# Kernel tuning notes

Hardware: AMD Instinct MI355X
Metric: run time of the kernel (lower is better)

The kernel has to match this reference:

```python
import jax, jax.numpy as jnp
import numpy as np

HEADS = 8
DIM_HEAD = 64
QUERY_DIM = 512
INNER = HEADS * DIM_HEAD
DIAG_OFFSET = 1
T_TEMP = 1.0
NEG_INF = -1e9  # used via -inf below; kept for clarity


def setup_inputs() -> dict:
    key = jax.random.key(0)
    ks = jax.random.split(key, 8)
    b, s, f = 2, 2048, 16
    x = jax.random.normal(ks[0], (b, s, f, QUERY_DIM), dtype=jnp.float32)
    pos_bias = jax.random.normal(ks[1], (HEADS, f, f), dtype=jnp.float32)
    w_scale = 0.02
    Wq = jax.random.normal(ks[2], (QUERY_DIM, INNER), dtype=jnp.float32) * w_scale
    Wk = jax.random.normal(ks[3], (QUERY_DIM, INNER), dtype=jnp.float32) * w_scale
    Wv = jax.random.normal(ks[4], (QUERY_DIM, INNER), dtype=jnp.float32) * w_scale
    Wo = jax.random.normal(ks[5], (INNER, QUERY_DIM), dtype=jnp.float32) * w_scale
    bo = jax.random.normal(ks[6], (QUERY_DIM,), dtype=jnp.float32) * w_scale
    return {"x": x, "pos_bias": pos_bias, "Wq": Wq, "Wk": Wk, "Wv": Wv, "Wo": Wo, "bo": bo}


def reference(x, pos_bias, Wq, Wk, Wv, Wo, bo):
    # x: [b, s, f, c] -- temporal attention over the frame axis f per spatial token
    b, s, f, _ = x.shape
    scale = DIM_HEAD ** -0.5
    q = (x @ Wq).reshape(b, s, f, HEADS, DIM_HEAD)
    k = (x @ Wk).reshape(b, s, f, HEADS, DIM_HEAD)
    v = (x @ Wv).reshape(b, s, f, HEADS, DIM_HEAD)
    # scores over frames: [b, s, h, f_q, f_k]
    w = jnp.einsum('bsihd,bsjhd->bshij', q * scale, k)
    w = w + pos_bias[None, None]  # [h, f, f] relative position bias
    # attend_prev_only causal mask (strict, diag_offset=1)
    causal = jnp.triu(jnp.ones((f, f), dtype=jnp.float32), k=DIAG_OFFSET)
    w = w + jnp.where(causal == 1.0, -jnp.inf, 0.0)
    # faithful to source: subtract row max, then softmax with temperature
    w = w - jax.lax.stop_gradient(jnp.max(w, axis=-1, keepdims=True))
    p = jax.nn.softmax(w.astype(jnp.float32) / T_TEMP, axis=-1).astype(w.dtype)
    out = jnp.einsum('bshij,bsjhd->bsihd', p, v).reshape(b, s, f, INNER)
    return out @ Wo + bo
```

## Files before the change

kernel.cpp:

```cpp
#include <hip/hip_runtime.h>

typedef unsigned short u16;
typedef __attribute__((ext_vector_type(8))) unsigned short u16x8;
typedef __attribute__((ext_vector_type(8))) __bf16 bf16x8;
typedef __attribute__((ext_vector_type(4))) float f32x4;

#define M_ROWS 65536
#define KDIM   512
#define NKT    8

typedef __attribute__((address_space(1))) const void gconst_void;
typedef __attribute__((address_space(3))) void lds_void;

static __device__ __forceinline__ u16 f2bf(float f) {
  unsigned u = __builtin_bit_cast(unsigned, f);
  u += 0x7FFFu + ((u >> 16) & 1u);
  return (u16)(u >> 16);
}

static __device__ __forceinline__ f32x4 mfma_bf16(u16x8 a, u16x8 b, f32x4 c) {
  return __builtin_amdgcn_mfma_f32_16x16x32_bf16(
      __builtin_bit_cast(bf16x8, a), __builtin_bit_cast(bf16x8, b), c, 0, 0, 0);
}

__global__ void conv_x(const float* __restrict__ x, u16* __restrict__ xb) {
  const size_t t = (size_t)blockIdx.x * 256 + threadIdx.x;
  f32x4 a = *(const f32x4*)(x + t * 8);
  f32x4 b = *(const f32x4*)(x + t * 8 + 4);
  u16x8 w;
#pragma unroll
  for (int e = 0; e < 4; ++e) { w[e] = f2bf(a[e]); w[e + 4] = f2bf(b[e]); }
  *(u16x8*)(xb + t * 8) = w;
}

__global__ void convW_qkv_t(const float* __restrict__ Wq, const float* __restrict__ Wk,
                            const float* __restrict__ Wv, u16* __restrict__ Wt) {
  __shared__ float tile[32][33];
  const int bn = blockIdx.x * 32;
  const int bk = blockIdx.y * 32;
  const int tx = threadIdx.x & 31, ty = threadIdx.x >> 5;
  const float* W = (bn < 512) ? Wq : ((bn < 1024) ? Wk : Wv);
  const int coln = bn & 511;
#pragma unroll
  for (int r = 0; r < 32; r += 8)
    tile[ty + r][tx] = W[(size_t)(bk + ty + r) * 512 + coln + tx];
  __syncthreads();
#pragma unroll
  for (int r = 0; r < 32; r += 8)
    Wt[(size_t)(bn + ty + r) * 512 + bk + tx] = f2bf(tile[tx][ty + r]);
}

__global__ void convWo_t(const float* __restrict__ Wo, u16* __restrict__ Wt) {
  __shared__ float tile[32][33];
  const int bn = blockIdx.x * 32;
  const int bk = blockIdx.y * 32;
  const int tx = threadIdx.x & 31, ty = threadIdx.x >> 5;
#pragma unroll
  for (int r = 0; r < 32; r += 8)
    tile[ty + r][tx] = Wo[(size_t)(bk + ty + r) * 512 + bn + tx];
  __syncthreads();
#pragma unroll
  for (int r = 0; r < 32; r += 8)
    Wt[(size_t)(bn + ty + r) * 512 + bk + tx] = f2bf(tile[tx][ty + r]);
}

__global__ __launch_bounds__(512, 4)
void gemm_qkv_attn(const u16* __restrict__ A, const u16* __restrict__ Wt,
                   const float* __restrict__ pos_bias, u16* __restrict__ attnbuf) {
  __shared__ __attribute__((aligned(16))) u16 smem[40960];
  u16* Ab   = smem;
  u16* Bb   = smem + 16384;
  u16* qkvT = smem;
  u16* Pl   = smem + 25600;

  const int tid  = threadIdx.x;
  const int lane = tid & 63;
  const int wid  = tid >> 6;
  const int wm   = wid >> 2;
  const int wn   = wid & 3;
  const int lg   = lane >> 4;
  const int lc   = lane & 15;
  const int srow = lane >> 3;
  const int sg   = (lane & 7) ^ srow;

  const int nwg  = gridDim.x;
  const int cpx  = nwg >> 3;
  const int flat = blockIdx.x;
  const int swz  = (flat & 7) * cpx + (flat >> 3);
  const int mt   = swz >> 3;
  const int h    = swz & 7;
  const int row0 = mt * 128;

  auto stageA = [&](int buf, int unit, int kt) {
    const int rl = unit * 64 + wid * 8;
    const u16* src = A + (size_t)(row0 + rl + srow) * KDIM + kt * 64 + sg * 8;
    __builtin_amdgcn_global_load_lds((gconst_void*)src,
                                     (lds_void*)&Ab[buf * 8192 + rl * 64], 16, 0, 0);
  };
  auto stageB = [&](int buf, int unit, int kt) {
    const int rl = unit * 64 + wid * 8;
    const int grow = unit * 512 + h * 64 + wid * 8 + srow;
    const u16* src = Wt + (size_t)grow * KDIM + kt * 64 + sg * 8;
    __builtin_amdgcn_global_load_lds((gconst_void*)src,
                                     (lds_void*)&Bb[buf * 12288 + rl * 64], 16, 0, 0);
  };

  f32x4 acc[4][3];
#pragma unroll
  for (int mi = 0; mi < 4; ++mi)
#pragma unroll
    for (int ni = 0; ni < 3; ++ni) acc[mi][ni] = (f32x4){0.f, 0.f, 0.f, 0.f};

  stageA(0, 0, 0); stageA(0, 1, 0);
  stageB(0, 0, 0); stageB(0, 1, 0); stageB(0, 2, 0);
  asm volatile("s_waitcnt vmcnt(0)" ::: "memory");
  __builtin_amdgcn_s_barrier();

  for (int t = 0; t < NKT; ++t) {
    const int  c   = t & 1;
    const bool pre = (t + 1) < NKT;

    if (pre) {
      stageA(c ^ 1, 0, t + 1); stageA(c ^ 1, 1, t + 1);
      stageB(c ^ 1, 0, t + 1); stageB(c ^ 1, 1, t + 1); stageB(c ^ 1, 2, t + 1);
    }

#pragma unroll
    for (int ks = 0; ks < 2; ++ks) {
      const int gsw = ((ks * 4 + lg) ^ (lc & 7)) << 3;
      u16x8 bfr[3], af[4];
#pragma unroll
      for (int ni = 0; ni < 3; ++ni)
        bfr[ni] = *(const u16x8*)&Bb[c * 12288 + (wn * 48 + ni * 16 + lc) * 64 + gsw];
#pragma unroll
      for (int i = 0; i < 4; ++i)
        af[i] = *(const u16x8*)&Ab[c * 8192 + (wm * 64 + i * 16 + lc) * 64 + gsw];
#pragma unroll
      for (int i = 0; i < 4; ++i)
#pragma unroll
        for (int ni = 0; ni < 3; ++ni)
          acc[i][ni] = mfma_bf16(af[i], bfr[ni], acc[i][ni]);
    }

    asm volatile("s_waitcnt vmcnt(0)" ::: "memory");
    __builtin_amdgcn_s_barrier();
  }

#pragma unroll
  for (int mi = 0; mi < 4; ++mi)
#pragma unroll
    for (int ni = 0; ni < 3; ++ni) {
      const int col = wn * 48 + ni * 16 + lc;
      const int rb  = wm * 64 + mi * 16 + lg * 4;
#pragma unroll
      for (int r = 0; r < 4; ++r)
        qkvT[(rb + r) * 200 + col] = f2bf(acc[mi][ni][r]);
    }
  __syncthreads();

  const float scale = 0.125f;
  const f32x4 zf = {0.f, 0.f, 0.f, 0.f};
  const int rb = wid * 16;
  const int qb = (rb + lc) * 200;

  u16x8 aq0 = *(const u16x8*)&qkvT[qb + 0  + lg * 8];
  u16x8 aq1 = *(const u16x8*)&qkvT[qb + 32 + lg * 8];
  u16x8 bk0 = *(const u16x8*)&qkvT[qb + 64 + lg * 8];
  u16x8 bk1 = *(const u16x8*)&qkvT[qb + 96 + lg * 8];
  f32x4 s = mfma_bf16(aq0, bk0, zf);
  s = mfma_bf16(aq1, bk1, s);

  const int pb = wid * 256;
#pragma unroll
  for (int r = 0; r < 4; ++r) {
    const int i = lg * 4 + r;
    float sv = s[r] * scale + pos_bias[h * 256 + i * 16 + lc];
    if (lc > i) sv = -1e30f;
    float m = sv;
#pragma unroll
    for (int off = 8; off >= 1; off >>= 1) m = fmaxf(m, __shfl_xor(m, off));
    float e = __expf(sv - m);
    float sm = e;
#pragma unroll
    for (int off = 8; off >= 1; off >>= 1) sm += __shfl_xor(sm, off);
    Pl[pb + i * 16 + lc] = f2bf(e / sm);
  }
  asm volatile("s_waitcnt lgkmcnt(0)" ::: "memory");

  u16x8 ap = {0, 0, 0, 0, 0, 0, 0, 0};
  if (lane < 32) ap = *(const u16x8*)&Pl[pb + lc * 16 + lg * 8];

#pragma unroll
  for (int nd = 0; nd < 4; ++nd) {
    u16x8 bv = {0, 0, 0, 0, 0, 0, 0, 0};
    if (lane < 32) {
#pragma unroll
      for (int jj = 0; jj < 8; ++jj) {
        const int j = lg * 8 + jj;
        bv[jj] = qkvT[(rb + j) * 200 + 128 + nd * 16 + lc];
      }
    }
    f32x4 o = mfma_bf16(ap, bv, zf);
#pragma unroll
    for (int r = 0; r < 4; ++r) {
      const int i = lg * 4 + r;
      attnbuf[(size_t)(row0 + rb + i) * 512 + h * 64 + nd * 16 + lc] = f2bf(o[r]);
    }
  }
}

__global__ __launch_bounds__(512, 4)
void gemm_out(const u16* __restrict__ A, const u16* __restrict__ Bt,
              float* __restrict__ C, const float* __restrict__ bias) {
  __shared__ __attribute__((aligned(16))) u16 smem[32768];
  u16* Ab = smem;
  u16* Bb = smem + 16384;

  const int tid  = threadIdx.x;
  const int lane = tid & 63;
  const int wid  = tid >> 6;
  const int wm   = wid >> 2;
  const int wn   = wid & 3;
  const int lg   = lane >> 4;
  const int lc   = lane & 15;
  const int srow = lane >> 3;
  const int sg   = (lane & 7) ^ srow;

  const int nwg  = gridDim.x;
  const int cpx  = nwg >> 3;
  const int flat = blockIdx.x;
  const int swz  = (flat & 7) * cpx + (flat >> 3);
  const int mt   = swz >> 2;
  const int nt   = swz & 3;
  const int row0 = mt * 128, col0 = nt * 128;

  auto stageA = [&](int buf, int unit, int kt) {
    const int rl = unit * 64 + wid * 8;
    const u16* src = A + (size_t)(row0 + rl + srow) * KDIM + kt * 64 + sg * 8;
    __builtin_amdgcn_global_load_lds((gconst_void*)src,
                                     (lds_void*)&Ab[buf * 8192 + rl * 64], 16, 0, 0);
  };
  auto stageB = [&](int buf, int unit, int kt) {
    const int rl = unit * 64 + wid * 8;
    const u16* src = Bt + (size_t)(col0 + rl + srow) * KDIM + kt * 64 + sg * 8;
    __builtin_amdgcn_global_load_lds((gconst_void*)src,
                                     (lds_void*)&Bb[buf * 8192 + rl * 64], 16, 0, 0);
  };

  f32x4 acc[4][2];
#pragma unroll
  for (int mi = 0; mi < 4; ++mi)
#pragma unroll
    for (int ni = 0; ni < 2; ++ni) acc[mi][ni] = (f32x4){0.f, 0.f, 0.f, 0.f};

  stageA(0, 0, 0); stageA(0, 1, 0);
  stageB(0, 0, 0); stageB(0, 1, 0);
  asm volatile("s_waitcnt vmcnt(0)" ::: "memory");
  __builtin_amdgcn_s_barrier();

  for (int t = 0; t < NKT; ++t) {
    const int  c   = t & 1;
    const bool pre = (t + 1) < NKT;

    if (pre) {
      stageA(c ^ 1, 0, t + 1); stageA(c ^ 1, 1, t + 1);
      stageB(c ^ 1, 0, t + 1); stageB(c ^ 1, 1, t + 1);
    }

#pragma unroll
    for (int ks = 0; ks < 2; ++ks) {
      const int gsw = ((ks * 4 + lg) ^ (lc & 7)) << 3;
      u16x8 bfr[2], af[4];
#pragma unroll
      for (int ni = 0; ni < 2; ++ni)
        bfr[ni] = *(const u16x8*)&Bb[c * 8192 + (wn * 32 + ni * 16 + lc) * 64 + gsw];
#pragma unroll
      for (int i = 0; i < 4; ++i)
        af[i] = *(const u16x8*)&Ab[c * 8192 + (wm * 64 + i * 16 + lc) * 64 + gsw];
#pragma unroll
      for (int i = 0; i < 4; ++i)
#pragma unroll
        for (int ni = 0; ni < 2; ++ni)
          acc[i][ni] = mfma_bf16(af[i], bfr[ni], acc[i][ni]);
    }

    asm volatile("s_waitcnt vmcnt(0)" ::: "memory");
    __builtin_amdgcn_s_barrier();
  }

  const int gmb = row0 + wm * 64;
  const int gnb = col0 + wn * 32;
#pragma unroll
  for (int mi = 0; mi < 4; ++mi)
#pragma unroll
    for (int ni = 0; ni < 2; ++ni) {
      const int gm = gmb + mi * 16 + lg * 4;
      const int gn = gnb + ni * 16 + lc;
      const float bv = bias[gn];
      f32x4 v = acc[mi][ni];
#pragma unroll
      for (int r = 0; r < 4; ++r) C[(size_t)(gm + r) * 512 + gn] = v[r] + bv;
    }
}

extern "C" void kernel_launch(void* const* d_in, const int* in_sizes, int n_in,
                              void* d_out, int out_size, void* d_ws, size_t ws_size,
                              hipStream_t stream) {
  const float* x        = (const float*)d_in[0];
  const float* pos_bias = (const float*)d_in[1];
  const float* Wq       = (const float*)d_in[2];
  const float* Wk       = (const float*)d_in[3];
  const float* Wv       = (const float*)d_in[4];
  const float* Wo       = (const float*)d_in[5];
  const float* bo       = (const float*)d_in[6];
  float* out            = (float*)d_out;

  u16* xb      = (u16*)d_ws;
  u16* attnbuf = xb + (size_t)M_ROWS * 512;
  u16* Wo_t    = attnbuf + (size_t)M_ROWS * 512;
  u16* Wqkv_t  = (u16*)d_out;

  conv_x<<<dim3(M_ROWS * KDIM / (256 * 8)), dim3(256), 0, stream>>>(x, xb);
  convW_qkv_t<<<dim3(48, 16), dim3(256), 0, stream>>>(Wq, Wk, Wv, Wqkv_t);
  gemm_qkv_attn<<<dim3(4096), dim3(512), 0, stream>>>(xb, Wqkv_t, pos_bias, attnbuf);
  convWo_t<<<dim3(16, 16), dim3(256), 0, stream>>>(Wo, Wo_t);
  gemm_out<<<dim3(2048), dim3(512), 0, stream>>>(attnbuf, Wo_t, out, bo);
}
```

Baseline: 210.5 us.

## Load weight fragments directly from global memory instead of staging in LDS

```diff
diff --git a/kernel.cpp b/kernel.cpp
--- a/kernel.cpp
+++ b/kernel.cpp
@@ -67,9 +67,8 @@
 __global__ __launch_bounds__(512, 4)
 void gemm_qkv_attn(const u16* __restrict__ A, const u16* __restrict__ Wt,
                    const float* __restrict__ pos_bias, u16* __restrict__ attnbuf) {
-  __shared__ __attribute__((aligned(16))) u16 smem[40960];
+  __shared__ __attribute__((aligned(16))) u16 smem[27648];
   u16* Ab   = smem;
-  u16* Bb   = smem + 16384;
   u16* qkvT = smem;
   u16* Pl   = smem + 25600;
 
@@ -97,13 +96,14 @@
     __builtin_amdgcn_global_load_lds((gconst_void*)src,
                                      (lds_void*)&Ab[buf * 8192 + rl * 64], 16, 0, 0);
   };
-  auto stageB = [&](int buf, int unit, int kt) {
-    const int rl = unit * 64 + wid * 8;
-    const int grow = unit * 512 + h * 64 + wid * 8 + srow;
-    const u16* src = Wt + (size_t)grow * KDIM + kt * 64 + sg * 8;
-    __builtin_amdgcn_global_load_lds((gconst_void*)src,
-                                     (lds_void*)&Bb[buf * 12288 + rl * 64], 16, 0, 0);
-  };
+
+  const u16* Bw[3];
+#pragma unroll
+  for (int ni = 0; ni < 3; ++ni) {
+    const int n    = wn * 48 + ni * 16 + lc;
+    const int grow = (n >> 6) * 512 + h * 64 + (n & 63);
+    Bw[ni] = Wt + (size_t)grow * KDIM;
+  }
 
   f32x4 acc[4][3];
 #pragma unroll
@@ -112,7 +112,6 @@
     for (int ni = 0; ni < 3; ++ni) acc[mi][ni] = (f32x4){0.f, 0.f, 0.f, 0.f};
 
   stageA(0, 0, 0); stageA(0, 1, 0);
-  stageB(0, 0, 0); stageB(0, 1, 0); stageB(0, 2, 0);
   asm volatile("s_waitcnt vmcnt(0)" ::: "memory");
   __builtin_amdgcn_s_barrier();
 
@@ -120,10 +119,7 @@
     const int  c   = t & 1;
     const bool pre = (t + 1) < NKT;
 
-    if (pre) {
-      stageA(c ^ 1, 0, t + 1); stageA(c ^ 1, 1, t + 1);
-      stageB(c ^ 1, 0, t + 1); stageB(c ^ 1, 1, t + 1); stageB(c ^ 1, 2, t + 1);
-    }
+    if (pre) { stageA(c ^ 1, 0, t + 1); stageA(c ^ 1, 1, t + 1); }
 
 #pragma unroll
     for (int ks = 0; ks < 2; ++ks) {
@@ -131,7 +127,7 @@
       u16x8 bfr[3], af[4];
 #pragma unroll
       for (int ni = 0; ni < 3; ++ni)
-        bfr[ni] = *(const u16x8*)&Bb[c * 12288 + (wn * 48 + ni * 16 + lc) * 64 + gsw];
+        bfr[ni] = *(const u16x8*)(Bw[ni] + t * 64 + ks * 32 + lg * 8);
 #pragma unroll
       for (int i = 0; i < 4; ++i)
         af[i] = *(const u16x8*)&Ab[c * 8192 + (wm * 64 + i * 16 + lc) * 64 + gsw];
@@ -209,12 +205,11 @@
   }
 }
 
-__global__ __launch_bounds__(512, 4)
+__global__ __launch_bounds__(512, 6)
 void gemm_out(const u16* __restrict__ A, const u16* __restrict__ Bt,
               float* __restrict__ C, const float* __restrict__ bias) {
-  __shared__ __attribute__((aligned(16))) u16 smem[32768];
+  __shared__ __attribute__((aligned(16))) u16 smem[16384];
   u16* Ab = smem;
-  u16* Bb = smem + 16384;
 
   const int tid  = threadIdx.x;
   const int lane = tid & 63;
@@ -240,12 +235,11 @@
     __builtin_amdgcn_global_load_lds((gconst_void*)src,
                                      (lds_void*)&Ab[buf * 8192 + rl * 64], 16, 0, 0);
   };
-  auto stageB = [&](int buf, int unit, int kt) {
-    const int rl = unit * 64 + wid * 8;
-    const u16* src = Bt + (size_t)(col0 + rl + srow) * KDIM + kt * 64 + sg * 8;
-    __builtin_amdgcn_global_load_lds((gconst_void*)src,
-                                     (lds_void*)&Bb[buf * 8192 + rl * 64], 16, 0, 0);
-  };
+
+  const u16* Bw[2];
+#pragma unroll
+  for (int ni = 0; ni < 2; ++ni)
+    Bw[ni] = Bt + (size_t)(col0 + wn * 32 + ni * 16 + lc) * KDIM;
 
   f32x4 acc[4][2];
 #pragma unroll
@@ -254,7 +248,6 @@
     for (int ni = 0; ni < 2; ++ni) acc[mi][ni] = (f32x4){0.f, 0.f, 0.f, 0.f};
 
   stageA(0, 0, 0); stageA(0, 1, 0);
-  stageB(0, 0, 0); stageB(0, 1, 0);
   asm volatile("s_waitcnt vmcnt(0)" ::: "memory");
   __builtin_amdgcn_s_barrier();
 
@@ -262,10 +255,7 @@
     const int  c   = t & 1;
     const bool pre = (t + 1) < NKT;
 
-    if (pre) {
-      stageA(c ^ 1, 0, t + 1); stageA(c ^ 1, 1, t + 1);
-      stageB(c ^ 1, 0, t + 1); stageB(c ^ 1, 1, t + 1);
-    }
+    if (pre) { stageA(c ^ 1, 0, t + 1); stageA(c ^ 1, 1, t + 1); }
 
 #pragma unroll
     for (int ks = 0; ks < 2; ++ks) {
@@ -273,7 +263,7 @@
       u16x8 bfr[2], af[4];
 #pragma unroll
       for (int ni = 0; ni < 2; ++ni)
-        bfr[ni] = *(const u16x8*)&Bb[c * 8192 + (wn * 32 + ni * 16 + lc) * 64 + gsw];
+        bfr[ni] = *(const u16x8*)(Bw[ni] + t * 64 + ks * 32 + lg * 8);
 #pragma unroll
       for (int i = 0; i < 4; ++i)
         af[i] = *(const u16x8*)&Ab[c * 8192 + (wm * 64 + i * 16 + lc) * 64 + gsw];
```

New measurement: 346.3 us. 64.5% more time.

## Load QKV weight fragments directly into registers instead of staging in LDS

Applied to the files above, without the earlier changes.

```diff
diff --git a/kernel.cpp b/kernel.cpp
--- a/kernel.cpp
+++ b/kernel.cpp
@@ -67,9 +67,8 @@
 __global__ __launch_bounds__(512, 4)
 void gemm_qkv_attn(const u16* __restrict__ A, const u16* __restrict__ Wt,
                    const float* __restrict__ pos_bias, u16* __restrict__ attnbuf) {
-  __shared__ __attribute__((aligned(16))) u16 smem[40960];
+  __shared__ __attribute__((aligned(16))) u16 smem[27648];
   u16* Ab   = smem;
-  u16* Bb   = smem + 16384;
   u16* qkvT = smem;
   u16* Pl   = smem + 25600;
 
@@ -97,13 +96,14 @@
     __builtin_amdgcn_global_load_lds((gconst_void*)src,
                                      (lds_void*)&Ab[buf * 8192 + rl * 64], 16, 0, 0);
   };
-  auto stageB = [&](int buf, int unit, int kt) {
-    const int rl = unit * 64 + wid * 8;
-    const int grow = unit * 512 + h * 64 + wid * 8 + srow;
-    const u16* src = Wt + (size_t)grow * KDIM + kt * 64 + sg * 8;
-    __builtin_amdgcn_global_load_lds((gconst_void*)src,
-                                     (lds_void*)&Bb[buf * 12288 + rl * 64], 16, 0, 0);
-  };
+
+  const u16* Bw[3];
+#pragma unroll
+  for (int ni = 0; ni < 3; ++ni) {
+    const int n    = wn * 48 + ni * 16 + lc;
+    const int grow = (n >> 6) * 512 + h * 64 + (n & 63);
+    Bw[ni] = Wt + (size_t)grow * KDIM;
+  }
 
   f32x4 acc[4][3];
 #pragma unroll
@@ -111,8 +111,14 @@
 #pragma unroll
     for (int ni = 0; ni < 3; ++ni) acc[mi][ni] = (f32x4){0.f, 0.f, 0.f, 0.f};
 
+  u16x8 bA[6], bB[6];
+
   stageA(0, 0, 0); stageA(0, 1, 0);
-  stageB(0, 0, 0); stageB(0, 1, 0); stageB(0, 2, 0);
+#pragma unroll
+  for (int ni = 0; ni < 3; ++ni)
+#pragma unroll
+    for (int ks = 0; ks < 2; ++ks)
+      bA[ni * 2 + ks] = *(const u16x8*)(Bw[ni] + 0 * 64 + ks * 32 + lg * 8);
   asm volatile("s_waitcnt vmcnt(0)" ::: "memory");
   __builtin_amdgcn_s_barrier();
 
@@ -122,16 +128,17 @@
 
     if (pre) {
       stageA(c ^ 1, 0, t + 1); stageA(c ^ 1, 1, t + 1);
-      stageB(c ^ 1, 0, t + 1); stageB(c ^ 1, 1, t + 1); stageB(c ^ 1, 2, t + 1);
+#pragma unroll
+      for (int ni = 0; ni < 3; ++ni)
+#pragma unroll
+        for (int ks = 0; ks < 2; ++ks)
+          bB[ni * 2 + ks] = *(const u16x8*)(Bw[ni] + (t + 1) * 64 + ks * 32 + lg * 8);
     }
 
 #pragma unroll
     for (int ks = 0; ks < 2; ++ks) {
       const int gsw = ((ks * 4 + lg) ^ (lc & 7)) << 3;
-      u16x8 bfr[3], af[4];
-#pragma unroll
-      for (int ni = 0; ni < 3; ++ni)
-        bfr[ni] = *(const u16x8*)&Bb[c * 12288 + (wn * 48 + ni * 16 + lc) * 64 + gsw];
+      u16x8 af[4];
 #pragma unroll
       for (int i = 0; i < 4; ++i)
         af[i] = *(const u16x8*)&Ab[c * 8192 + (wm * 64 + i * 16 + lc) * 64 + gsw];
@@ -139,9 +146,13 @@
       for (int i = 0; i < 4; ++i)
 #pragma unroll
         for (int ni = 0; ni < 3; ++ni)
-          acc[i][ni] = mfma_bf16(af[i], bfr[ni], acc[i][ni]);
-    }
-
+          acc[i][ni] = mfma_bf16(af[i], bA[ni * 2 + ks], acc[i][ni]);
+    }
+
+    if (pre) {
+#pragma unroll
+      for (int u = 0; u < 6; ++u) bA[u] = bB[u];
+    }
     asm volatile("s_waitcnt vmcnt(0)" ::: "memory");
     __builtin_amdgcn_s_barrier();
   }
```

Result: slower. 327.9 us (+55.8%).
